# Optimization experiments

Hardware: AMD Instinct MI355X
Metric: run time of the kernel (lower is better)

## Reference

```python
import jax, jax.numpy as jnp
import numpy as np

D = 6
EPS = 1e-5


def layer_norm(x, w, b):
    m = jnp.mean(x, axis=-1, keepdims=True)
    v = jnp.mean(jnp.square(x - m), axis=-1, keepdims=True)
    return (x - m) * jax.lax.rsqrt(v + EPS) * w + b


def setup_inputs() -> dict:
    key = jax.random.key(0)
    ks = jax.random.split(key, 8)
    B, S = 8192, 128
    scale = 0.2
    return {
        "x": jax.random.normal(ks[0], (B, S, D), jnp.float32),
        "ln1_w": jnp.ones((D,), jnp.float32),
        "ln1_b": jnp.zeros((D,), jnp.float32),
        "wqkv": jax.random.normal(ks[1], (D, 3 * D), jnp.float32) * scale,
        "bqkv": jnp.zeros((3 * D,), jnp.float32),
        "wo": jax.random.normal(ks[2], (D, D), jnp.float32) * scale,
        "bo": jnp.zeros((D,), jnp.float32),
        "ln2_w": jnp.ones((D,), jnp.float32),
        "ln2_b": jnp.zeros((D,), jnp.float32),
        "w1": jax.random.normal(ks[3], (D, D), jnp.float32) * scale,
        "b1": jnp.zeros((D,), jnp.float32),
        "w2": jax.random.normal(ks[4], (D, D), jnp.float32) * scale,
        "b2": jnp.zeros((D,), jnp.float32),
    }


def reference(x, ln1_w, ln1_b, wqkv, bqkv, wo, bo, ln2_w, ln2_b, w1, b1, w2, b2):
    B, S, _ = x.shape
    # --- attention sub-block: x = x + attn(ln1(x)) ---
    h = layer_norm(x, ln1_w, ln1_b)                      # [B,S,D]
    qkv = h @ wqkv + bqkv                                # [B,S,3D]
    q, k, v = jnp.split(qkv, 3, axis=-1)
    scores = jnp.einsum('bqd,bkd->bqk', q, k) / jnp.sqrt(jnp.asarray(D, x.dtype))
    causal = jnp.tril(jnp.ones((S, S), bool))            # [S,S]
    scores = jnp.where(causal, scores, jnp.asarray(-1e9, x.dtype))
    attn = jax.nn.softmax(scores, axis=-1)               # [B,S,S]
    o = jnp.einsum('bqk,bkd->bqd', attn, v) @ wo + bo
    x = x + o
    # --- FFN sub-block: x = x + W2 @ gelu(W1 @ ln2(x)) ---
    h2 = layer_norm(x, ln2_w, ln2_b)
    ff = jax.nn.gelu(h2 @ w1 + b1, approximate=False) @ w2 + b2
    return x + ff
```

## Files before the change

### kernel.cpp

```cpp
#include <hip/hip_runtime.h>
#include <cmath>


typedef float    v2f  __attribute__((ext_vector_type(2)));
typedef uint32_t u2   __attribute__((ext_vector_type(2)));
typedef short    s8v  __attribute__((ext_vector_type(8)));
typedef float    f16v __attribute__((ext_vector_type(16)));

constexpr int D = 6;
constexpr int S = 128;
#define EPS 1e-5f
#define RSQRT_D 0.4082482904638631f
#define LOG2E   1.4426950408889634f

#define EXP2F(x) __builtin_amdgcn_exp2f(x)
#define RCPF(x)  __builtin_amdgcn_rcpf(x)
#define PKFMA(a, b, c) __builtin_elementwise_fma((a), (b), (c))

union U4 { uint32_t u[4]; u2 h[2]; s8v v; };

__device__ __forceinline__ uint32_t pkbf(float hi, float lo) {
    return __builtin_amdgcn_perm(__builtin_bit_cast(uint32_t, hi),
                                 __builtin_bit_cast(uint32_t, lo),
                                 0x07060302u);
}
__device__ __forceinline__ uint16_t bf16t(float x) {
    return (uint16_t)(__builtin_bit_cast(uint32_t, x) >> 16);
}

__global__ __launch_bounds__(S, 4) void txblock_kernel(
    const float* __restrict__ x,
    const float* __restrict__ ln1_w, const float* __restrict__ ln1_b,
    const float* __restrict__ wqkv,  const float* __restrict__ bqkv,
    const float* __restrict__ wo,    const float* __restrict__ bo,
    const float* __restrict__ ln2_w, const float* __restrict__ ln2_b,
    const float* __restrict__ w1,    const float* __restrict__ b1,
    const float* __restrict__ w2,    const float* __restrict__ b2,
    float* __restrict__ out)
{
    __shared__ uint32_t qlds[S][10];
    __shared__ uint32_t klds[S][10];
    __shared__ uint16_t vt[8][S + 8];
    __shared__ float    obuf[S][10];

    const int b = blockIdx.x;
    const int s = threadIdx.x;
    const float* xrow = x + ((size_t)b * S + s) * D;
    float*      orow = out + ((size_t)b * S + s) * D;

    v2f xv01 = ((const v2f*)xrow)[0];
    v2f xv23 = ((const v2f*)xrow)[1];
    v2f xv45 = ((const v2f*)xrow)[2];
    float xv[D] = {xv01[0], xv01[1], xv23[0], xv23[1], xv45[0], xv45[1]};

    float m = 0.f;
    #pragma unroll
    for (int d = 0; d < D; ++d) m += xv[d];
    m *= (1.0f / D);
    float var = 0.f;
    #pragma unroll
    for (int d = 0; d < D; ++d) { float t = xv[d] - m; var += t * t; }
    var *= (1.0f / D);
    float rstd = rsqrtf(var + EPS);
    float h1[D];
    #pragma unroll
    for (int d = 0; d < D; ++d)
        h1[d] = (xv[d] - m) * rstd * ln1_w[d] + ln1_b[d];

    v2f aq[3], ak[3], av[3];
    #pragma unroll
    for (int jp = 0; jp < 3; ++jp) {
        aq[jp] = ((const v2f*)bqkv)[jp];
        ak[jp] = ((const v2f*)(bqkv + D))[jp];
        av[jp] = ((const v2f*)(bqkv + 2 * D))[jp];
    }
    #pragma unroll
    for (int d = 0; d < D; ++d) {
        const float* wrow = wqkv + d * 3 * D;
        v2f hd = {h1[d], h1[d]};
        #pragma unroll
        for (int jp = 0; jp < 3; ++jp) {
            aq[jp] = PKFMA(hd, ((const v2f*)wrow)[jp], aq[jp]);
            ak[jp] = PKFMA(hd, ((const v2f*)(wrow + D))[jp], ak[jp]);
            av[jp] = PKFMA(hd, ((const v2f*)(wrow + 2 * D))[jp], av[jp]);
        }
    }
    const v2f qscale = {RSQRT_D * LOG2E, RSQRT_D * LOG2E};

    #pragma unroll
    for (int jp = 0; jp < 3; ++jp) {
        v2f qs = aq[jp] * qscale;
        qlds[s][jp] = pkbf(qs[1], qs[0]);
        klds[s][jp] = pkbf(ak[jp][1], ak[jp][0]);
    }
    #pragma unroll
    for (int c = 3; c < 8; ++c) { qlds[s][c] = 0; klds[s][c] = 0; }
    vt[0][s] = bf16t(av[0][0]);
    vt[1][s] = bf16t(av[0][1]);
    vt[2][s] = bf16t(av[1][0]);
    vt[3][s] = bf16t(av[1][1]);
    vt[4][s] = bf16t(av[2][0]);
    vt[5][s] = bf16t(av[2][1]);
    vt[6][s] = 0x3F80;
    vt[7][s] = 0;
    __syncthreads();

    const int wv = s >> 6;
    const int ln = s & 31;
    const int hw = (s >> 5) & 1;
    const int ne = (ln < 6) ? ln : 6;

    const int mt0 = wv ? 1 : 0;
    const int mt1 = wv ? 2 : 3;

    #pragma unroll
    for (int pass = 0; pass < 2; ++pass) {
        const int mt = pass ? mt1 : mt0;
        U4 qf;
        {
            const u2* p = (const u2*)&qlds[mt * 32 + ln][hw * 4];
            qf.h[0] = p[0]; qf.h[1] = p[1];
        }
        f16v O = (f16v)(0.0f);
        for (int kt = 0; kt <= mt; ++kt) {
            U4 kf;
            {
                const u2* p = (const u2*)&klds[kt * 32 + ln][hw * 4];
                kf.h[0] = p[0]; kf.h[1] = p[1];
            }
            f16v c1 = __builtin_amdgcn_mfma_f32_32x32x16_bf16(
                          kf.v, qf.v, (f16v)(0.0f), 0, 0, 0);
            uint32_t pk[8], rp[8];
            #pragma unroll
            for (int t = 0; t < 8; ++t) {
                float p0 = EXP2F(c1[2 * t]);
                float p1 = EXP2F(c1[2 * t + 1]);
                if (kt == mt) {
                    const int j0 = ((2 * t) & 3) + 8 * ((2 * t) >> 2) + 4 * hw;
                    const int j1 = ((2 * t + 1) & 3) + 8 * ((2 * t + 1) >> 2) + 4 * hw;
                    p0 = (j0 > ln) ? 0.0f : p0;
                    p1 = (j1 > ln) ? 0.0f : p1;
                }
                pk[t] = pkbf(p1, p0);
                rp[t] = (uint32_t)__shfl_xor((int)pk[t], 32);
            }
            U4 a1, a2;
            a1.u[0] = hw ? rp[2] : pk[0];
            a1.u[1] = hw ? rp[3] : pk[1];
            a1.u[2] = hw ? pk[2] : rp[0];
            a1.u[3] = hw ? pk[3] : rp[1];
            a2.u[0] = hw ? rp[6] : pk[4];
            a2.u[1] = hw ? rp[7] : pk[5];
            a2.u[2] = hw ? pk[6] : rp[4];
            a2.u[3] = hw ? pk[7] : rp[5];
            s8v vb1 = *(const s8v*)&vt[ne][kt * 32 + hw * 8];
            s8v vb2 = *(const s8v*)&vt[ne][kt * 32 + 16 + hw * 8];
            O = __builtin_amdgcn_mfma_f32_32x32x16_bf16(a1.v, vb1, O, 0, 0, 0);
            O = __builtin_amdgcn_mfma_f32_32x32x16_bf16(a2.v, vb2, O, 0, 0, 0);
        }
        if (ln < 7) {
            #pragma unroll
            for (int r = 0; r < 16; ++r) {
                int row = (r & 3) + 8 * (r >> 2) + 4 * hw;
                obuf[mt * 32 + row][ln] = O[r];
            }
        }
    }
    __syncthreads();

    v2f o01 = *(const v2f*)&obuf[s][0];
    v2f o23 = *(const v2f*)&obuf[s][2];
    v2f o45 = *(const v2f*)&obuf[s][4];
    float invl = RCPF(obuf[s][6]);
    v2f il = {invl, invl};
    o01 *= il; o23 *= il; o45 *= il;
    float av6[D] = {o01[0], o01[1], o23[0], o23[1], o45[0], o45[1]};

    v2f xvp[3] = {xv01, xv23, xv45};
    v2f x2p[3];
    #pragma unroll
    for (int dp = 0; dp < 3; ++dp) {
        v2f o = ((const v2f*)bo)[dp];
        #pragma unroll
        for (int e = 0; e < D; ++e) {
            v2f we = ((const v2f*)(wo + e * D))[dp];
            v2f ae = {av6[e], av6[e]};
            o = PKFMA(ae, we, o);
        }
        x2p[dp] = o + xvp[dp];
    }
    float x2[D] = {x2p[0][0], x2p[0][1], x2p[1][0], x2p[1][1], x2p[2][0], x2p[2][1]};

    float m2 = 0.f;
    #pragma unroll
    for (int d = 0; d < D; ++d) m2 += x2[d];
    m2 *= (1.0f / D);
    float var2 = 0.f;
    #pragma unroll
    for (int d = 0; d < D; ++d) { float t = x2[d] - m2; var2 += t * t; }
    var2 *= (1.0f / D);
    float rstd2 = rsqrtf(var2 + EPS);
    float h2[D];
    #pragma unroll
    for (int d = 0; d < D; ++d)
        h2[d] = (x2[d] - m2) * rstd2 * ln2_w[d] + ln2_b[d];

    v2f ap[3];
    #pragma unroll
    for (int jp = 0; jp < 3; ++jp) {
        v2f a = ((const v2f*)b1)[jp];
        #pragma unroll
        for (int d = 0; d < D; ++d) {
            v2f wd = ((const v2f*)(w1 + d * D))[jp];
            v2f hd = {h2[d], h2[d]};
            a = PKFMA(hd, wd, a);
        }
        ap[jp] = a;
    }
    float g[D];
    #pragma unroll
    for (int j = 0; j < D; ++j) {
        float a = ap[j >> 1][j & 1];
        float t  = a * a;
        float in = fmaf(0.044715f * t, a, a);
        float e  = EXP2F(in * -2.3022229f);
        float r  = RCPF(1.0f + e);
        g[j] = a * r;
    }
    #pragma unroll
    for (int dp = 0; dp < 3; ++dp) {
        v2f a = ((const v2f*)b2)[dp];
        #pragma unroll
        for (int e = 0; e < D; ++e) {
            v2f we = ((const v2f*)(w2 + e * D))[dp];
            v2f ge = {g[e], g[e]};
            a = PKFMA(ge, we, a);
        }
        ((v2f*)orow)[dp] = x2p[dp] + a;
    }
}

extern "C" void kernel_launch(void* const* d_in, const int* in_sizes, int n_in,
                              void* d_out, int out_size, void* d_ws, size_t ws_size,
                              hipStream_t stream) {
    const float* x     = (const float*)d_in[0];
    const float* ln1_w = (const float*)d_in[1];
    const float* ln1_b = (const float*)d_in[2];
    const float* wqkv  = (const float*)d_in[3];
    const float* bqkv  = (const float*)d_in[4];
    const float* wo    = (const float*)d_in[5];
    const float* bo    = (const float*)d_in[6];
    const float* ln2_w = (const float*)d_in[7];
    const float* ln2_b = (const float*)d_in[8];
    const float* w1    = (const float*)d_in[9];
    const float* b1    = (const float*)d_in[10];
    const float* w2    = (const float*)d_in[11];
    const float* b2    = (const float*)d_in[12];
    float* out = (float*)d_out;

    const int B = in_sizes[0] / (S * D);
    txblock_kernel<<<B, S, 0, stream>>>(x, ln1_w, ln1_b, wqkv, bqkv, wo, bo,
                                        ln2_w, ln2_b, w1, b1, w2, b2, out);
}
```

Measured before the change: 118.6 us.

## Switch causal attention from 32x32 to 16x16 MFMA tiles

Replaces the 32x32x16 bf16 MFMA attention with 16x16x16 tiles. Each wave handles four 16-row query tiles in a balanced pattern (0,3,4,7 and 1,2,5,6). Because the probability tile now maps straight into the A-operand layout, the cross-half shuffles and select logic are gone. Smaller causal tiles also skip more of the masked upper triangle and shrink the LDS footprint of the Q and K buffers. In exchange there are more MFMA issues and loop iterations, and there is an inline-asm fallback with fixed nops if the builtin is missing.

```diff
diff --git a/kernel.cpp b/kernel.cpp
--- a/kernel.cpp
+++ b/kernel.cpp
@@ -3,9 +3,9 @@
 
 
 typedef float    v2f  __attribute__((ext_vector_type(2)));
+typedef float    f4v  __attribute__((ext_vector_type(4)));
+typedef short    s4v  __attribute__((ext_vector_type(4)));
 typedef uint32_t u2   __attribute__((ext_vector_type(2)));
-typedef short    s8v  __attribute__((ext_vector_type(8)));
-typedef float    f16v __attribute__((ext_vector_type(16)));
 
 constexpr int D = 6;
 constexpr int S = 128;
@@ -17,7 +17,7 @@
 #define RCPF(x)  __builtin_amdgcn_rcpf(x)
 #define PKFMA(a, b, c) __builtin_elementwise_fma((a), (b), (c))
 
-union U4 { uint32_t u[4]; u2 h[2]; s8v v; };
+union UA { uint32_t u[2]; u2 h; s4v v; };
 
 __device__ __forceinline__ uint32_t pkbf(float hi, float lo) {
     return __builtin_amdgcn_perm(__builtin_bit_cast(uint32_t, hi),
@@ -26,6 +26,18 @@
 }
 __device__ __forceinline__ uint16_t bf16t(float x) {
     return (uint16_t)(__builtin_bit_cast(uint32_t, x) >> 16);
+}
+
+__device__ __forceinline__ f4v mfma16(s4v a, s4v b, f4v c) {
+#if __has_builtin(__builtin_amdgcn_mfma_f32_16x16x16bf16_1k)
+    return __builtin_amdgcn_mfma_f32_16x16x16bf16_1k(a, b, c, 0, 0, 0);
+#else
+    f4v d;
+    asm volatile("v_mfma_f32_16x16x16_bf16 %0, %1, %2, %3\n\t"
+                 "s_nop 7\n\ts_nop 2"
+                 : "=v"(d) : "v"(a), "v"(b), "v"(c));
+    return d;
+#endif
 }
 
 __global__ __launch_bounds__(S, 4) void txblock_kernel(
@@ -38,8 +50,8 @@
     const float* __restrict__ w2,    const float* __restrict__ b2,
     float* __restrict__ out)
 {
-    __shared__ uint32_t qlds[S][10];
-    __shared__ uint32_t klds[S][10];
+    __shared__ uint32_t qlds[S][6];
+    __shared__ uint32_t klds[S][6];
     __shared__ uint16_t vt[8][S + 8];
     __shared__ float    obuf[S][10];
 
@@ -93,8 +105,8 @@
         qlds[s][jp] = pkbf(qs[1], qs[0]);
         klds[s][jp] = pkbf(ak[jp][1], ak[jp][0]);
     }
-    #pragma unroll
-    for (int c = 3; c < 8; ++c) { qlds[s][c] = 0; klds[s][c] = 0; }
+    qlds[s][3] = 0; qlds[s][4] = 0; qlds[s][5] = 0;
+    klds[s][3] = 0; klds[s][4] = 0; klds[s][5] = 0;
     vt[0][s] = bf16t(av[0][0]);
     vt[1][s] = bf16t(av[0][1]);
     vt[2][s] = bf16t(av[1][0]);
@@ -105,65 +117,42 @@
     vt[7][s] = 0;
     __syncthreads();
 
-    const int wv = s >> 6;
-    const int ln = s & 31;
-    const int hw = (s >> 5) & 1;
-    const int ne = (ln < 6) ? ln : 6;
-
-    const int mt0 = wv ? 1 : 0;
-    const int mt1 = wv ? 2 : 3;
-
-    #pragma unroll
-    for (int pass = 0; pass < 2; ++pass) {
-        const int mt = pass ? mt1 : mt0;
-        U4 qf;
-        {
-            const u2* p = (const u2*)&qlds[mt * 32 + ln][hw * 4];
-            qf.h[0] = p[0]; qf.h[1] = p[1];
-        }
-        f16v O = (f16v)(0.0f);
-        for (int kt = 0; kt <= mt; ++kt) {
-            U4 kf;
-            {
-                const u2* p = (const u2*)&klds[kt * 32 + ln][hw * 4];
-                kf.h[0] = p[0]; kf.h[1] = p[1];
+    const int wv  = s >> 6;
+    const int l15 = s & 15;
+    const int lq  = (s >> 4) & 3;
+    const int aoff = (lq < 2) ? lq * 8 : 16;
+    const int vne  = (l15 < 7) ? l15 : 7;
+
+    #pragma unroll
+    for (int i = 0; i < 4; ++i) {
+        static const int QT0[4] = {0, 3, 4, 7};
+        static const int QT1[4] = {1, 2, 5, 6};
+        const int qt = wv ? QT1[i] : QT0[i];
+        UA qf; qf.h = *(const u2*)((const char*)&qlds[qt * 16 + l15][0] + aoff);
+        f4v O = {0.f, 0.f, 0.f, 0.f};
+        for (int jt = 0; jt <= qt; ++jt) {
+            UA kf; kf.h = *(const u2*)((const char*)&klds[jt * 16 + l15][0] + aoff);
+            f4v c = mfma16(kf.v, qf.v, (f4v){0.f, 0.f, 0.f, 0.f});
+            float p0 = EXP2F(c[0]);
+            float p1 = EXP2F(c[1]);
+            float p2 = EXP2F(c[2]);
+            float p3 = EXP2F(c[3]);
+            if (jt == qt) {
+                p0 = (lq * 4 + 0 > l15) ? 0.f : p0;
+                p1 = (lq * 4 + 1 > l15) ? 0.f : p1;
+                p2 = (lq * 4 + 2 > l15) ? 0.f : p2;
+                p3 = (lq * 4 + 3 > l15) ? 0.f : p3;
             }
-            f16v c1 = __builtin_amdgcn_mfma_f32_32x32x16_bf16(
-                          kf.v, qf.v, (f16v)(0.0f), 0, 0, 0);
-            uint32_t pk[8], rp[8];
+            UA pa;
+            pa.u[0] = pkbf(p1, p0);
+            pa.u[1] = pkbf(p3, p2);
+            UA vf; vf.h = *(const u2*)&vt[vne][jt * 16 + lq * 4];
+            O = mfma16(pa.v, vf.v, O);
+        }
+        if (l15 < 7) {
             #pragma unroll
-            for (int t = 0; t < 8; ++t) {
-                float p0 = EXP2F(c1[2 * t]);
-                float p1 = EXP2F(c1[2 * t + 1]);
-                if (kt == mt) {
-                    const int j0 = ((2 * t) & 3) + 8 * ((2 * t) >> 2) + 4 * hw;
-                    const int j1 = ((2 * t + 1) & 3) + 8 * ((2 * t + 1) >> 2) + 4 * hw;
-                    p0 = (j0 > ln) ? 0.0f : p0;
-                    p1 = (j1 > ln) ? 0.0f : p1;
-                }
-                pk[t] = pkbf(p1, p0);
-                rp[t] = (uint32_t)__shfl_xor((int)pk[t], 32);
-            }
-            U4 a1, a2;
-            a1.u[0] = hw ? rp[2] : pk[0];
-            a1.u[1] = hw ? rp[3] : pk[1];
-            a1.u[2] = hw ? pk[2] : rp[0];
-            a1.u[3] = hw ? pk[3] : rp[1];
-            a2.u[0] = hw ? rp[6] : pk[4];
-            a2.u[1] = hw ? rp[7] : pk[5];
-            a2.u[2] = hw ? pk[6] : rp[4];
-            a2.u[3] = hw ? pk[7] : rp[5];
-            s8v vb1 = *(const s8v*)&vt[ne][kt * 32 + hw * 8];
-            s8v vb2 = *(const s8v*)&vt[ne][kt * 32 + 16 + hw * 8];
-            O = __builtin_amdgcn_mfma_f32_32x32x16_bf16(a1.v, vb1, O, 0, 0, 0);
-            O = __builtin_amdgcn_mfma_f32_32x32x16_bf16(a2.v, vb2, O, 0, 0, 0);
-        }
-        if (ln < 7) {
-            #pragma unroll
-            for (int r = 0; r < 16; ++r) {
-                int row = (r & 3) + 8 * (r >> 2) + 4 * hw;
-                obuf[mt * 32 + row][ln] = O[r];
-            }
+            for (int r = 0; r < 4; ++r)
+                obuf[qt * 16 + lq * 4 + r][l15] = O[r];
         }
     }
     __syncthreads();
```

Result: no change. 116.6 us (-1.7%).
